# Kernel optimization log

Hardware: AMD Instinct MI355X
Metric: run time of the kernel (lower is better)

Reference implementation:

```python
import jax, jax.numpy as jnp
import numpy as np

SCALE = 4.0  # InputEmbedding scale


def setup_inputs() -> dict:
    key = jax.random.key(0)
    ks = jax.random.split(key, 16)
    T_obs, T_pred, N, E, H = 9, 12, 16384, 64, 128
    n_scenes = 512  # N / 32 tracks per scene
    inp = {
        "observed": jax.random.normal(ks[0], (T_obs, N, 2), jnp.float32),
        "prediction": jax.random.normal(ks[1], (T_pred, N, 2), jnp.float32),
        "goals": jax.random.normal(ks[2], (N, 2), jnp.float32),
        "batch_split": jnp.arange(0, N + 1, N // n_scenes, dtype=jnp.int64),
        # InputEmbedding: Linear(2 -> E)
        "W_emb": jax.random.normal(ks[3], (E, 2), jnp.float32) * 0.5,
        "b_emb": jax.random.normal(ks[4], (E,), jnp.float32) * 0.1,
        # LSTMCell(E -> H)
        "W_ih": jax.random.normal(ks[5], (4 * H, E), jnp.float32) * 0.08,
        "W_hh": jax.random.normal(ks[6], (4 * H, H), jnp.float32) * 0.08,
        "b_ih": jax.random.normal(ks[7], (4 * H,), jnp.float32) * 0.05,
        "b_hh": jax.random.normal(ks[8], (4 * H,), jnp.float32) * 0.05,
        # real_classifier MLP: [H, H/2, H/4, 1], ReLU after every Linear
        "W1": jax.random.normal(ks[9], (H // 2, H), jnp.float32) * 0.08,
        "b1": jnp.zeros((H // 2,), jnp.float32),
        "W2": jax.random.normal(ks[10], (H // 4, H // 2), jnp.float32) * 0.12,
        "b2": jnp.zeros((H // 4,), jnp.float32),
        "W3": jax.random.normal(ks[11], (1, H // 4), jnp.float32) * 0.2,
        "b3": jnp.zeros((1,), jnp.float32),
    }
    return inp


def _lstm_cell(x, h, c, W_ih, W_hh, b_ih, b_hh):
    gates = x @ W_ih.T + b_ih + h @ W_hh.T + b_hh  # [N, 4H]
    i, f, g, o = jnp.split(gates, 4, axis=-1)
    i = jax.nn.sigmoid(i)
    f = jax.nn.sigmoid(f)
    o = jax.nn.sigmoid(o)
    g = jnp.tanh(g)
    c2 = f * c + i * g
    h2 = o * jnp.tanh(c2)
    return h2, c2


def reference(observed, prediction, goals, batch_split,
              W_emb, b_emb, W_ih, W_hh, b_ih, b_hh,
              W1, b1, W2, b2, W3, b3):
    # pool=None, goal_flag=False -> step is: NaN-mask, velocity embed, LSTMCell,
    # masked write-back of (h, c) for valid tracks only.
    obs = jnp.concatenate([observed, prediction], axis=0)  # [T, N, 2]
    N = obs.shape[1]
    H = W_hh.shape[1]

    def step(carry, o12):
        h, c = carry
        o1, o2 = o12
        mask = ~(jnp.isnan(o1[:, 0]) | jnp.isnan(o2[:, 0]))  # [N]
        vel = jnp.where(mask[:, None], o2 - o1, 0.0)  # [N, 2]
        emb = (vel * SCALE) @ W_emb.T + b_emb  # [N, E]
        h2, c2 = _lstm_cell(emb, h, c, W_ih, W_hh, b_ih, b_hh)
        h = jnp.where(mask[:, None], h2, h)
        c = jnp.where(mask[:, None], c2, c)
        return (h, c), None

    h0 = jnp.zeros((N, H), obs.dtype)
    c0 = jnp.zeros((N, H), obs.dtype)
    (h, _c), _ = jax.lax.scan(step, (h0, c0), (obs[:-1], obs[1:]))

    primary = h[batch_split[:-1]]  # [batch_size, H]
    # make_mlp with relu appends ReLU after every Linear, including the last.
    x = jax.nn.relu(primary @ W1.T + b1)
    x = jax.nn.relu(x @ W2.T + b2)
    scores = jax.nn.relu(x @ W3.T + b3)  # [batch_size, 1]
    return scores
```

## Files before the change

### kernel.cpp

```cpp
#include <hip/hip_runtime.h>
#include <math.h>

#define SCALE 4.0f
#define H 128
#define E 64
#define NS 4
#define TMAX 32

#define WS_LO_OFF  131072
#define WS_UC_OFF  262144

typedef __attribute__((ext_vector_type(8))) short short8;
typedef __attribute__((ext_vector_type(4))) float f32x4;

__device__ __forceinline__ bool is_nanf(float x) {
    return (__float_as_uint(x) & 0x7fffffffu) > 0x7f800000u;
}
__device__ __forceinline__ float rcpf(float x) { return __builtin_amdgcn_rcpf(x); }
__device__ __forceinline__ float sigm(float x) { return rcpf(1.0f + __expf(-x)); }
__device__ __forceinline__ float tanhfast(float x) {
    return fmaf(2.0f, rcpf(1.0f + __expf(-2.0f * x)), -1.0f);
}
__device__ __forceinline__ unsigned short bfhi(float f) {
    unsigned u = __float_as_uint(f);
    unsigned r = u + 0x7fffu + ((u >> 16) & 1u);
    return (unsigned short)(r >> 16);
}
__device__ __forceinline__ float bff(unsigned short h) {
    return __uint_as_float(((unsigned)h) << 16);
}

__global__ __launch_bounds__(256)
void prep_kernel(const float* __restrict__ W_hh,
                 const float* __restrict__ W_ih,
                 const float* __restrict__ W_emb,
                 const float* __restrict__ b_emb,
                 const float* __restrict__ b_ih,
                 const float* __restrict__ b_hh,
                 char* __restrict__ ws)
{
    const int gid = blockIdx.x * 256 + threadIdx.x;
    if (gid < 8192) {
        const int lane = gid & 63;
        const int kb   = (gid >> 6) & 3;
        const int q    = (gid >> 8) & 3;
        const int w    = gid >> 10;
        const int mt   = q * 8 + w;
        const int row  = mt * 16 + (lane & 15);
        const int col0 = kb * 32 + (lane >> 4) * 8;
        const float* p = W_hh + (size_t)row * H + col0;
        short8 h8, l8;
        #pragma unroll
        for (int j = 0; j < 8; ++j) {
            const float f = p[j];
            const unsigned short hb = bfhi(f);
            h8[j] = (short)hb;
            l8[j] = (short)bfhi(f - bff(hb));
        }
        *(short8*)(ws + (size_t)gid * 16)             = h8;
        *(short8*)(ws + WS_LO_OFF + (size_t)gid * 16) = l8;
    } else if (gid < 8192 + 512) {
        const int r = gid - 8192;
        const float* wr = W_ih + (size_t)r * E;
        float s0 = 0.f, s1 = 0.f, sc = 0.f;
        #pragma unroll 8
        for (int k = 0; k < E; ++k) {
            const float wv = wr[k];
            s0 += wv * W_emb[2 * k + 0];
            s1 += wv * W_emb[2 * k + 1];
            sc += wv * b_emb[k];
        }
        f32x4 v = {s0, s1, sc + b_ih[r] + b_hh[r], 0.0f};
        *(f32x4*)(ws + WS_UC_OFF + (size_t)r * 16) = v;
    }
}

__global__ __launch_bounds__(512, 2)
void lstm_disc_kernel(
    const float* __restrict__ observed,
    const float* __restrict__ prediction,
    const int* __restrict__ batch_split,
    const char* __restrict__ ws,
    const float* __restrict__ W1, const float* __restrict__ b1,
    const float* __restrict__ W2, const float* __restrict__ b2,
    const float* __restrict__ W3, const float* __restrict__ b3,
    float* __restrict__ out,
    int N, int T_obs, int T_total, int n_scenes)
{
    __shared__ __align__(16) short hb_hi[2][4][16][8];
    __shared__ __align__(16) short hb_lo[2][4][16][8];
    __shared__ float h32[NS][H];
    __shared__ float px[NS][TMAX], py[NS][TMAX];
    __shared__ float aA[NS][TMAX], bA[NS][TMAX];
    __shared__ int   mA[NS][TMAX];
    __shared__ float x1s[NS][H / 2];
    __shared__ float x2s[NS][H / 4];

    const int tid  = threadIdx.x;
    const int wave = tid >> 6;
    const int lane = tid & 63;
    const int ln15 = lane & 15;
    const int g4   = lane >> 4;
    const int es   = ln15 & 3;
    const int ea   = ln15 >> 2;
    const int eu   = wave * 16 + g4 * 4 + ea;
    const int sc0  = blockIdx.x * NS;

    if (tid < NS * TMAX) {
        const int s = tid >> 5, t = tid & 31;
        const int scene = sc0 + s;
        const int agent = (scene < n_scenes) ? batch_split[scene] : 0;
        if (t < T_total) {
            const float* src = (t < T_obs)
                ? (observed   + (size_t)t           * N * 2)
                : (prediction + (size_t)(t - T_obs) * N * 2);
            px[s][t] = src[(size_t)agent * 2 + 0];
            py[s][t] = src[(size_t)agent * 2 + 1];
        }
    }
    {
        int* zh = (int*)hb_hi;
        int* zl = (int*)hb_lo;
        if (tid < 512) { zh[tid] = 0; zl[tid] = 0; }
    }
    __syncthreads();

    if (tid < NS * TMAX) {
        const int s = tid >> 5, t = tid & 31;
        if (t < T_total - 1) {
            const bool m = !(is_nanf(px[s][t]) || is_nanf(px[s][t + 1]));
            aA[s][t] = m ? SCALE * (px[s][t + 1] - px[s][t]) : 0.0f;
            bA[s][t] = m ? SCALE * (py[s][t + 1] - py[s][t]) : 0.0f;
            mA[s][t] = m ? 1 : 0;
        }
    }

    short8 ahi[4][4], alo[4][4];
    #pragma unroll
    for (int q = 0; q < 4; ++q) {
        #pragma unroll
        for (int kb = 0; kb < 4; ++kb) {
            const size_t idx = ((size_t)((wave * 4 + q) * 4 + kb) * 64 + lane) * 16;
            ahi[q][kb] = *(const short8*)(ws + idx);
            alo[q][kb] = *(const short8*)(ws + WS_LO_OFF + idx);
        }
    }

    float U0r[4], U1r[4], Ccr[4];
    #pragma unroll
    for (int q = 0; q < 4; ++q) {
        const f32x4 v = *(const f32x4*)(ws + WS_UC_OFF + (size_t)(eu + q * H) * 16);
        U0r[q] = v[0]; U1r[q] = v[1]; Ccr[q] = v[2];
    }

    const int wb_kb = eu >> 5;
    const int wb_ln = ((eu >> 3) & 3) + 4 * es;
    const int wb_j  = eu & 7;

    float c_st = 0.0f, h_st = 0.0f;
    __syncthreads();

    for (int t = 0; t < T_total - 1; ++t) {
        const int rp = t & 1, wp = rp ^ 1;

        const float aa = aA[es][t];
        const float bb = bA[es][t];
        const int   mm = mA[es][t];

        short8 bhi[4], blo[4];
        #pragma unroll
        for (int kb = 0; kb < 4; ++kb) {
            bhi[kb] = *(const short8*)&hb_hi[rp][kb][g4 + 4 * es][0];
            blo[kb] = *(const short8*)&hb_lo[rp][kb][g4 + 4 * es][0];
        }

        f32x4 accA[4], accB[4];
        #pragma unroll
        for (int q = 0; q < 4; ++q) {
            accA[q] = (f32x4){0.f, 0.f, 0.f, 0.f};
            accB[q] = (f32x4){0.f, 0.f, 0.f, 0.f};
        }
        #pragma unroll
        for (int kb = 0; kb < 4; ++kb) {
            #pragma unroll
            for (int q = 0; q < 4; ++q)
                accA[q] = __builtin_amdgcn_mfma_f32_16x16x32_bf16(ahi[q][kb], bhi[kb], accA[q], 0, 0, 0);
        }
        #pragma unroll
        for (int kb = 0; kb < 4; ++kb) {
            #pragma unroll
            for (int q = 0; q < 4; ++q) {
                accA[q] = __builtin_amdgcn_mfma_f32_16x16x32_bf16(ahi[q][kb], blo[kb], accA[q], 0, 0, 0);
                accB[q] = __builtin_amdgcn_mfma_f32_16x16x32_bf16(alo[q][kb], bhi[kb], accB[q], 0, 0, 0);
            }
        }

        const float p0 = accA[0][ea] + accB[0][ea] + Ccr[0] + aa * U0r[0] + bb * U1r[0];
        const float p1 = accA[1][ea] + accB[1][ea] + Ccr[1] + aa * U0r[1] + bb * U1r[1];
        const float p2 = accA[2][ea] + accB[2][ea] + Ccr[2] + aa * U0r[2] + bb * U1r[2];
        const float p3 = accA[3][ea] + accB[3][ea] + Ccr[3] + aa * U0r[3] + bb * U1r[3];
        const float ig = sigm(p0);
        const float fg = sigm(p1);
        const float gg = tanhfast(p2);
        const float og = sigm(p3);
        const float c2 = fg * c_st + ig * gg;
        const float h2 = og * tanhfast(c2);
        if (mm) { c_st = c2; h_st = h2; }

        const unsigned short hhi = bfhi(h_st);
        const unsigned short hlo = bfhi(h_st - bff(hhi));
        hb_hi[wp][wb_kb][wb_ln][wb_j] = (short)hhi;
        hb_lo[wp][wb_kb][wb_ln][wb_j] = (short)hlo;
        if (t == T_total - 2) h32[es][eu] = h_st;

        __syncthreads();
    }

    if (tid < NS * (H / 2)) {
        const int s = tid >> 6, u = tid & 63;
        const float4* wr = (const float4*)(W1 + (size_t)u * H);
        const float4* hv = (const float4*)h32[s];
        float sum = b1[u];
        #pragma unroll
        for (int k = 0; k < H / 4; ++k) {
            const float4 w = wr[k], h = hv[k];
            sum += h.x * w.x + h.y * w.y + h.z * w.z + h.w * w.w;
        }
        x1s[s][u] = fmaxf(sum, 0.f);
    }
    __syncthreads();
    if (tid < NS * (H / 4)) {
        const int s = tid >> 5, u = tid & 31;
        const float4* wr = (const float4*)(W2 + (size_t)u * (H / 2));
        const float4* xv = (const float4*)x1s[s];
        float sum = b2[u];
        #pragma unroll
        for (int k = 0; k < H / 8; ++k) {
            const float4 w = wr[k], x = xv[k];
            sum += x.x * w.x + x.y * w.y + x.z * w.z + x.w * w.w;
        }
        x2s[s][u] = fmaxf(sum, 0.f);
    }
    __syncthreads();
    if (tid < NS) {
        const int scene = sc0 + tid;
        if (scene < n_scenes) {
            float sum = b3[0];
            #pragma unroll
            for (int k = 0; k < H / 4; ++k) sum += x2s[tid][k] * W3[k];
            out[scene] = fmaxf(sum, 0.f);
        }
    }
}

extern "C" void kernel_launch(void* const* d_in, const int* in_sizes, int n_in,
                              void* d_out, int out_size, void* d_ws, size_t ws_size,
                              hipStream_t stream) {
    const float* observed   = (const float*)d_in[0];
    const float* prediction = (const float*)d_in[1];
    const int*   batch_split = (const int*)d_in[3];
    const float* W_emb = (const float*)d_in[4];
    const float* b_emb = (const float*)d_in[5];
    const float* W_ih  = (const float*)d_in[6];
    const float* W_hh  = (const float*)d_in[7];
    const float* b_ih  = (const float*)d_in[8];
    const float* b_hh  = (const float*)d_in[9];
    const float* W1 = (const float*)d_in[10];
    const float* b1 = (const float*)d_in[11];
    const float* W2 = (const float*)d_in[12];
    const float* b2 = (const float*)d_in[13];
    const float* W3 = (const float*)d_in[14];
    const float* b3 = (const float*)d_in[15];
    float* out = (float*)d_out;

    const int N       = in_sizes[2] / 2;
    const int T_obs   = in_sizes[0] / (2 * N);
    const int T_total = T_obs + in_sizes[1] / (2 * N);
    const int n_scenes = in_sizes[3] - 1;

    prep_kernel<<<36, 256, 0, stream>>>(
        W_hh, W_ih, W_emb, b_emb, b_ih, b_hh, (char*)d_ws);

    const int nblocks = (n_scenes + NS - 1) / NS;
    lstm_disc_kernel<<<nblocks, 512, 0, stream>>>(
        observed, prediction, batch_split, (const char*)d_ws,
        W1, b1, W2, b2, W3, b3,
        out, N, T_obs, T_total, n_scenes);
}
```

Measured before the change: 118.1 us.

## Assign one scene per block and hoist weight-fragment loads before input gather

The LSTM kernel now runs one scene per block instead of packing four scenes into the MFMA column slots, launching n_scenes blocks. The goal is to spread the recurrence across more CUs, since the old 128-block grid left many of them idle. The workspace weight and bias register loads are also moved ahead of the trajectory gather so their latency overlaps. The trade-off is that the four MFMA columns now compute identical redundant work, and two 512-thread blocks per CU may contend for the matrix units.

```diff
diff --git a/kernel.cpp b/kernel.cpp
--- a/kernel.cpp
+++ b/kernel.cpp
@@ -4,7 +4,6 @@
 #define SCALE 4.0f
 #define H 128
 #define E 64
-#define NS 4
 #define TMAX 32
 
 #define WS_LO_OFF  131072
@@ -89,12 +88,12 @@
 {
     __shared__ __align__(16) short hb_hi[2][4][16][8];
     __shared__ __align__(16) short hb_lo[2][4][16][8];
-    __shared__ float h32[NS][H];
-    __shared__ float px[NS][TMAX], py[NS][TMAX];
-    __shared__ float aA[NS][TMAX], bA[NS][TMAX];
-    __shared__ int   mA[NS][TMAX];
-    __shared__ float x1s[NS][H / 2];
-    __shared__ float x2s[NS][H / 4];
+    __shared__ float h32[H];
+    __shared__ float px[TMAX], py[TMAX];
+    __shared__ float aA[TMAX], bA[TMAX];
+    __shared__ int   mA[TMAX];
+    __shared__ float x1s[H / 2];
+    __shared__ float x2s[H / 4];
 
     const int tid  = threadIdx.x;
     const int wave = tid >> 6;
@@ -104,18 +103,34 @@
     const int es   = ln15 & 3;
     const int ea   = ln15 >> 2;
     const int eu   = wave * 16 + g4 * 4 + ea;
-    const int sc0  = blockIdx.x * NS;
-
-    if (tid < NS * TMAX) {
-        const int s = tid >> 5, t = tid & 31;
-        const int scene = sc0 + s;
+    const int scene = blockIdx.x;
+
+    short8 ahi[4][4], alo[4][4];
+    #pragma unroll
+    for (int q = 0; q < 4; ++q) {
+        #pragma unroll
+        for (int kb = 0; kb < 4; ++kb) {
+            const size_t idx = ((size_t)((wave * 4 + q) * 4 + kb) * 64 + lane) * 16;
+            ahi[q][kb] = *(const short8*)(ws + idx);
+            alo[q][kb] = *(const short8*)(ws + WS_LO_OFF + idx);
+        }
+    }
+    float U0r[4], U1r[4], Ccr[4];
+    #pragma unroll
+    for (int q = 0; q < 4; ++q) {
+        const f32x4 v = *(const f32x4*)(ws + WS_UC_OFF + (size_t)(eu + q * H) * 16);
+        U0r[q] = v[0]; U1r[q] = v[1]; Ccr[q] = v[2];
+    }
+
+    if (tid < TMAX) {
+        const int t = tid;
         const int agent = (scene < n_scenes) ? batch_split[scene] : 0;
         if (t < T_total) {
             const float* src = (t < T_obs)
                 ? (observed   + (size_t)t           * N * 2)
                 : (prediction + (size_t)(t - T_obs) * N * 2);
-            px[s][t] = src[(size_t)agent * 2 + 0];
-            py[s][t] = src[(size_t)agent * 2 + 1];
+            px[t] = src[(size_t)agent * 2 + 0];
+            py[t] = src[(size_t)agent * 2 + 1];
         }
     }
     {
@@ -125,32 +140,14 @@
     }
     __syncthreads();
 
-    if (tid < NS * TMAX) {
-        const int s = tid >> 5, t = tid & 31;
+    if (tid < TMAX) {
+        const int t = tid;
         if (t < T_total - 1) {
-            const bool m = !(is_nanf(px[s][t]) || is_nanf(px[s][t + 1]));
-            aA[s][t] = m ? SCALE * (px[s][t + 1] - px[s][t]) : 0.0f;
-            bA[s][t] = m ? SCALE * (py[s][t + 1] - py[s][t]) : 0.0f;
-            mA[s][t] = m ? 1 : 0;
-        }
-    }
-
-    short8 ahi[4][4], alo[4][4];
-    #pragma unroll
-    for (int q = 0; q < 4; ++q) {
-        #pragma unroll
-        for (int kb = 0; kb < 4; ++kb) {
-            const size_t idx = ((size_t)((wave * 4 + q) * 4 + kb) * 64 + lane) * 16;
-            ahi[q][kb] = *(const short8*)(ws + idx);
-            alo[q][kb] = *(const short8*)(ws + WS_LO_OFF + idx);
-        }
-    }
-
-    float U0r[4], U1r[4], Ccr[4];
-    #pragma unroll
-    for (int q = 0; q < 4; ++q) {
-        const f32x4 v = *(const f32x4*)(ws + WS_UC_OFF + (size_t)(eu + q * H) * 16);
-        U0r[q] = v[0]; U1r[q] = v[1]; Ccr[q] = v[2];
+            const bool m = !(is_nanf(px[t]) || is_nanf(px[t + 1]));
+            aA[t] = m ? SCALE * (px[t + 1] - px[t]) : 0.0f;
+            bA[t] = m ? SCALE * (py[t + 1] - py[t]) : 0.0f;
+            mA[t] = m ? 1 : 0;
+        }
     }
 
     const int wb_kb = eu >> 5;
@@ -163,9 +160,9 @@
     for (int t = 0; t < T_total - 1; ++t) {
         const int rp = t & 1, wp = rp ^ 1;
 
-        const float aa = aA[es][t];
-        const float bb = bA[es][t];
-        const int   mm = mA[es][t];
+        const float aa = aA[t];
+        const float bb = bA[t];
+        const int   mm = mA[t];
 
         short8 bhi[4], blo[4];
         #pragma unroll
@@ -211,45 +208,42 @@
         const unsigned short hlo = bfhi(h_st - bff(hhi));
         hb_hi[wp][wb_kb][wb_ln][wb_j] = (short)hhi;
         hb_lo[wp][wb_kb][wb_ln][wb_j] = (short)hlo;
-        if (t == T_total - 2) h32[es][eu] = h_st;
+        if (t == T_total - 2 && es == 0) h32[eu] = h_st;
 
         __syncthreads();
     }
 
-    if (tid < NS * (H / 2)) {
-        const int s = tid >> 6, u = tid & 63;
+    if (tid < H / 2) {
+        const int u = tid;
         const float4* wr = (const float4*)(W1 + (size_t)u * H);
-        const float4* hv = (const float4*)h32[s];
+        const float4* hv = (const float4*)h32;
         float sum = b1[u];
         #pragma unroll
         for (int k = 0; k < H / 4; ++k) {
             const float4 w = wr[k], h = hv[k];
             sum += h.x * w.x + h.y * w.y + h.z * w.z + h.w * w.w;
         }
-        x1s[s][u] = fmaxf(sum, 0.f);
-    }
-    __syncthreads();
-    if (tid < NS * (H / 4)) {
-        const int s = tid >> 5, u = tid & 31;
+        x1s[u] = fmaxf(sum, 0.f);
+    }
+    __syncthreads();
+    if (tid < H / 4) {
+        const int u = tid;
         const float4* wr = (const float4*)(W2 + (size_t)u * (H / 2));
-        const float4* xv = (const float4*)x1s[s];
+        const float4* xv = (const float4*)x1s;
         float sum = b2[u];
         #pragma unroll
         for (int k = 0; k < H / 8; ++k) {
             const float4 w = wr[k], x = xv[k];
             sum += x.x * w.x + x.y * w.y + x.z * w.z + x.w * w.w;
         }
-        x2s[s][u] = fmaxf(sum, 0.f);
-    }
-    __syncthreads();
-    if (tid < NS) {
-        const int scene = sc0 + tid;
-        if (scene < n_scenes) {
-            float sum = b3[0];
-            #pragma unroll
-            for (int k = 0; k < H / 4; ++k) sum += x2s[tid][k] * W3[k];
-            out[scene] = fmaxf(sum, 0.f);
-        }
+        x2s[u] = fmaxf(sum, 0.f);
+    }
+    __syncthreads();
+    if (tid == 0 && scene < n_scenes) {
+        float sum = b3[0];
+        #pragma unroll
+        for (int k = 0; k < H / 4; ++k) sum += x2s[k] * W3[k];
+        out[scene] = fmaxf(sum, 0.f);
     }
 }
 
@@ -281,8 +275,7 @@
     prep_kernel<<<36, 256, 0, stream>>>(
         W_hh, W_ih, W_emb, b_emb, b_ih, b_hh, (char*)d_ws);
 
-    const int nblocks = (n_scenes + NS - 1) / NS;
-    lstm_disc_kernel<<<nblocks, 512, 0, stream>>>(
+    lstm_disc_kernel<<<n_scenes, 512, 0, stream>>>(
         observed, prediction, batch_split, (const char*)d_ws,
         W1, b1, W2, b2, W3, b3,
         out, N, T_obs, T_total, n_scenes);
```

Result: slower. 141.1 us (+19.5%).

## Switch recurrent MFMA to fp16 with split-h only, halve scenes per block

Applied to the files above, without the earlier changes.

Weights W_hh are stored as a single fp16 copy instead of a bf16 hi/lo pair. The hidden state is still split into fp16 hi/lo, so each step issues 32 MFMAs instead of 48. Scenes per block drop from 4 to 2, which doubles the grid to 256 blocks to fill more CUs, but the MFMA N dimension is now half redundant. Weight loads are hoisted before the input staging. The cost is lower weight precision from fp16 rounding of W_hh.

```diff
diff --git a/kernel.cpp b/kernel.cpp
--- a/kernel.cpp
+++ b/kernel.cpp
@@ -4,13 +4,12 @@
 #define SCALE 4.0f
 #define H 128
 #define E 64
-#define NS 4
+#define NS 2
 #define TMAX 32
 
-#define WS_LO_OFF  131072
-#define WS_UC_OFF  262144
-
-typedef __attribute__((ext_vector_type(8))) short short8;
+#define WS_UC_OFF  131072
+
+typedef _Float16 f16x8 __attribute__((ext_vector_type(8)));
 typedef __attribute__((ext_vector_type(4))) float f32x4;
 
 __device__ __forceinline__ bool is_nanf(float x) {
@@ -20,14 +19,6 @@
 __device__ __forceinline__ float sigm(float x) { return rcpf(1.0f + __expf(-x)); }
 __device__ __forceinline__ float tanhfast(float x) {
     return fmaf(2.0f, rcpf(1.0f + __expf(-2.0f * x)), -1.0f);
-}
-__device__ __forceinline__ unsigned short bfhi(float f) {
-    unsigned u = __float_as_uint(f);
-    unsigned r = u + 0x7fffu + ((u >> 16) & 1u);
-    return (unsigned short)(r >> 16);
-}
-__device__ __forceinline__ float bff(unsigned short h) {
-    return __uint_as_float(((unsigned)h) << 16);
 }
 
 __global__ __launch_bounds__(256)
@@ -49,16 +40,10 @@
         const int row  = mt * 16 + (lane & 15);
         const int col0 = kb * 32 + (lane >> 4) * 8;
         const float* p = W_hh + (size_t)row * H + col0;
-        short8 h8, l8;
-        #pragma unroll
-        for (int j = 0; j < 8; ++j) {
-            const float f = p[j];
-            const unsigned short hb = bfhi(f);
-            h8[j] = (short)hb;
-            l8[j] = (short)bfhi(f - bff(hb));
-        }
-        *(short8*)(ws + (size_t)gid * 16)             = h8;
-        *(short8*)(ws + WS_LO_OFF + (size_t)gid * 16) = l8;
+        f16x8 h8;
+        #pragma unroll
+        for (int j = 0; j < 8; ++j) h8[j] = (_Float16)p[j];
+        *(f16x8*)(ws + (size_t)gid * 16) = h8;
     } else if (gid < 8192 + 512) {
         const int r = gid - 8192;
         const float* wr = W_ih + (size_t)r * E;
@@ -87,8 +72,8 @@
     float* __restrict__ out,
     int N, int T_obs, int T_total, int n_scenes)
 {
-    __shared__ __align__(16) short hb_hi[2][4][16][8];
-    __shared__ __align__(16) short hb_lo[2][4][16][8];
+    __shared__ __align__(16) _Float16 hb_hi[2][4][8][8];
+    __shared__ __align__(16) _Float16 hb_lo[2][4][8][8];
     __shared__ float h32[NS][H];
     __shared__ float px[NS][TMAX], py[NS][TMAX];
     __shared__ float aA[NS][TMAX], bA[NS][TMAX];
@@ -102,9 +87,26 @@
     const int ln15 = lane & 15;
     const int g4   = lane >> 4;
     const int es   = ln15 & 3;
+    const int esc  = es & 1;
     const int ea   = ln15 >> 2;
     const int eu   = wave * 16 + g4 * 4 + ea;
     const int sc0  = blockIdx.x * NS;
+
+    f16x8 ahi[4][4];
+    #pragma unroll
+    for (int q = 0; q < 4; ++q) {
+        #pragma unroll
+        for (int kb = 0; kb < 4; ++kb) {
+            const size_t idx = ((size_t)((wave * 4 + q) * 4 + kb) * 64 + lane) * 16;
+            ahi[q][kb] = *(const f16x8*)(ws + idx);
+        }
+    }
+    float U0r[4], U1r[4], Ccr[4];
+    #pragma unroll
+    for (int q = 0; q < 4; ++q) {
+        const f32x4 v = *(const f32x4*)(ws + WS_UC_OFF + (size_t)(eu + q * H) * 16);
+        U0r[q] = v[0]; U1r[q] = v[1]; Ccr[q] = v[2];
+    }
 
     if (tid < NS * TMAX) {
         const int s = tid >> 5, t = tid & 31;
@@ -121,7 +123,7 @@
     {
         int* zh = (int*)hb_hi;
         int* zl = (int*)hb_lo;
-        if (tid < 512) { zh[tid] = 0; zl[tid] = 0; }
+        if (tid < 256) { zh[tid] = 0; zl[tid] = 0; }
     }
     __syncthreads();
 
@@ -135,27 +137,10 @@
         }
     }
 
-    short8 ahi[4][4], alo[4][4];
-    #pragma unroll
-    for (int q = 0; q < 4; ++q) {
-        #pragma unroll
-        for (int kb = 0; kb < 4; ++kb) {
-            const size_t idx = ((size_t)((wave * 4 + q) * 4 + kb) * 64 + lane) * 16;
-            ahi[q][kb] = *(const short8*)(ws + idx);
-            alo[q][kb] = *(const short8*)(ws + WS_LO_OFF + idx);
-        }
-    }
-
-    float U0r[4], U1r[4], Ccr[4];
-    #pragma unroll
-    for (int q = 0; q < 4; ++q) {
-        const f32x4 v = *(const f32x4*)(ws + WS_UC_OFF + (size_t)(eu + q * H) * 16);
-        U0r[q] = v[0]; U1r[q] = v[1]; Ccr[q] = v[2];
-    }
-
     const int wb_kb = eu >> 5;
-    const int wb_ln = ((eu >> 3) & 3) + 4 * es;
+    const int wb_ln = ((eu >> 3) & 3) + 4 * esc;
     const int wb_j  = eu & 7;
+    const bool wb_on = (es < 2);
 
     float c_st = 0.0f, h_st = 0.0f;
     __syncthreads();
@@ -163,42 +148,36 @@
     for (int t = 0; t < T_total - 1; ++t) {
         const int rp = t & 1, wp = rp ^ 1;
 
-        const float aa = aA[es][t];
-        const float bb = bA[es][t];
-        const int   mm = mA[es][t];
-
-        short8 bhi[4], blo[4];
+        const float aa = aA[esc][t];
+        const float bb = bA[esc][t];
+        const int   mm = mA[esc][t];
+
+        f16x8 bhi[4], blo[4];
         #pragma unroll
         for (int kb = 0; kb < 4; ++kb) {
-            bhi[kb] = *(const short8*)&hb_hi[rp][kb][g4 + 4 * es][0];
-            blo[kb] = *(const short8*)&hb_lo[rp][kb][g4 + 4 * es][0];
-        }
-
-        f32x4 accA[4], accB[4];
+            bhi[kb] = *(const f16x8*)&hb_hi[rp][kb][g4 + 4 * esc][0];
+            blo[kb] = *(const f16x8*)&hb_lo[rp][kb][g4 + 4 * esc][0];
+        }
+
+        f32x4 accH[4], accL[4];
         #pragma unroll
         for (int q = 0; q < 4; ++q) {
-            accA[q] = (f32x4){0.f, 0.f, 0.f, 0.f};
-            accB[q] = (f32x4){0.f, 0.f, 0.f, 0.f};
-        }
-        #pragma unroll
-        for (int kb = 0; kb < 4; ++kb) {
-            #pragma unroll
-            for (int q = 0; q < 4; ++q)
-                accA[q] = __builtin_amdgcn_mfma_f32_16x16x32_bf16(ahi[q][kb], bhi[kb], accA[q], 0, 0, 0);
+            accH[q] = (f32x4){0.f, 0.f, 0.f, 0.f};
+            accL[q] = (f32x4){0.f, 0.f, 0.f, 0.f};
         }
         #pragma unroll
         for (int kb = 0; kb < 4; ++kb) {
             #pragma unroll
             for (int q = 0; q < 4; ++q) {
-                accA[q] = __builtin_amdgcn_mfma_f32_16x16x32_bf16(ahi[q][kb], blo[kb], accA[q], 0, 0, 0);
-                accB[q] = __builtin_amdgcn_mfma_f32_16x16x32_bf16(alo[q][kb], bhi[kb], accB[q], 0, 0, 0);
+                accH[q] = __builtin_amdgcn_mfma_f32_16x16x32_f16(ahi[q][kb], bhi[kb], accH[q], 0, 0, 0);
+                accL[q] = __builtin_amdgcn_mfma_f32_16x16x32_f16(ahi[q][kb], blo[kb], accL[q], 0, 0, 0);
             }
         }
 
-        const float p0 = accA[0][ea] + accB[0][ea] + Ccr[0] + aa * U0r[0] + bb * U1r[0];
-        const float p1 = accA[1][ea] + accB[1][ea] + Ccr[1] + aa * U0r[1] + bb * U1r[1];
-        const float p2 = accA[2][ea] + accB[2][ea] + Ccr[2] + aa * U0r[2] + bb * U1r[2];
-        const float p3 = accA[3][ea] + accB[3][ea] + Ccr[3] + aa * U0r[3] + bb * U1r[3];
+        const float p0 = accH[0][ea] + accL[0][ea] + Ccr[0] + aa * U0r[0] + bb * U1r[0];
+        const float p1 = accH[1][ea] + accL[1][ea] + Ccr[1] + aa * U0r[1] + bb * U1r[1];
+        const float p2 = accH[2][ea] + accL[2][ea] + Ccr[2] + aa * U0r[2] + bb * U1r[2];
+        const float p3 = accH[3][ea] + accL[3][ea] + Ccr[3] + aa * U0r[3] + bb * U1r[3];
         const float ig = sigm(p0);
         const float fg = sigm(p1);
         const float gg = tanhfast(p2);
@@ -207,12 +186,13 @@
         const float h2 = og * tanhfast(c2);
         if (mm) { c_st = c2; h_st = h2; }
 
-        const unsigned short hhi = bfhi(h_st);
-        const unsigned short hlo = bfhi(h_st - bff(hhi));
-        hb_hi[wp][wb_kb][wb_ln][wb_j] = (short)hhi;
-        hb_lo[wp][wb_kb][wb_ln][wb_j] = (short)hlo;
-        if (t == T_total - 2) h32[es][eu] = h_st;
-
+        if (wb_on) {
+            const _Float16 hhi = (_Float16)h_st;
+            const _Float16 hlo = (_Float16)(h_st - (float)hhi);
+            hb_hi[wp][wb_kb][wb_ln][wb_j] = hhi;
+            hb_lo[wp][wb_kb][wb_ln][wb_j] = hlo;
+            if (t == T_total - 2) h32[esc][eu] = h_st;
+        }
         __syncthreads();
     }
 
@@ -278,7 +258,7 @@
     const int T_total = T_obs + in_sizes[1] / (2 * N);
     const int n_scenes = in_sizes[3] - 1;
 
-    prep_kernel<<<36, 256, 0, stream>>>(
+    prep_kernel<<<34, 256, 0, stream>>>(
         W_hh, W_ih, W_emb, b_emb, b_ih, b_hh, (char*)d_ws);
 
     const int nblocks = (n_scenes + NS - 1) / NS;
```

Measured after the change: 111.8 us. 1.06x faster.
